# Performance work log

Hardware: AMD Instinct MI355X
Metric: run time of the kernel (lower is better)

The kernel has to match this reference:

```python
import jax, jax.numpy as jnp
import numpy as np

# Inside algorithm for a binary TreeCRF over a complete binary tree in heap
# layout: node i has children 2i+1 and 2i+2; level of size n starts at index
# n-1. Leaves are the last (n_nodes+1)//2 entries of `emissions`.
#
# Original per-node math:
#   inside[p] = logsumexp_{i,j}( em[p] + trans[p,i] + left[i] + trans[p,j] + right[j] )
# which factorizes exactly as
#   inside[p] = em[p] + logsumexp_i(trans[p,i]+left[i]) + logsumexp_j(trans[p,j]+right[j])


def setup_inputs() -> dict:
    key = jax.random.key(0)
    k1, k2 = jax.random.split(key)
    n_leaves = 131072  # 2**17
    n_nodes = 2 * n_leaves - 1  # 262143
    L = 32
    emissions = jax.random.normal(k1, (n_nodes, L), dtype=jnp.float32)
    trans = jax.random.normal(k2, (L, L), dtype=jnp.float32)
    return {"emissions": emissions, "trans": trans}


def _child_contrib(trans, child):
    # child: [n, L] inside scores of children; trans: [L, L]
    # returns [n, L]: logsumexp_c(trans[p, c] + child[:, c])
    return jax.nn.logsumexp(trans[None, :, :] + child[:, None, :], axis=2)


def reference(emissions, trans):
    n_nodes = emissions.shape[0]
    n_leaves = (n_nodes + 1) // 2
    # leaf inside scores are just the leaf emissions
    scores = emissions[n_leaves - 1:]  # [n_leaves, L]
    level = n_leaves // 2
    while level >= 1:
        # children of node (level-1)+k are scores[2k] (left) and scores[2k+1] (right)
        left = scores[0::2]   # [level, L]
        right = scores[1::2]  # [level, L]
        em = emissions[level - 1: 2 * level - 1]  # [level, L]
        scores = em + _child_contrib(trans, left) + _child_contrib(trans, right)
        level //= 2
    return scores[0]  # root inside score, [L]
```

## Files before the change

### kernel.cpp

```cpp
#include <hip/hip_runtime.h>


typedef float f32x4 __attribute__((ext_vector_type(4)));
typedef short s16x8 __attribute__((ext_vector_type(8)));
typedef short s16x4 __attribute__((ext_vector_type(4)));

#define CSTR 40

__device__ __forceinline__ short f2bf(float f) {
    unsigned u = __builtin_bit_cast(unsigned, f);
    unsigned r = (u + 0x7fffu + ((u >> 16) & 1u)) >> 16;
    return (short)r;
}

__device__ __forceinline__ float max4(float4 v) {
    return fmaxf(fmaxf(v.x, v.y), fmaxf(v.z, v.w));
}

__device__ __forceinline__ void load_afrag(const float* __restrict__ trans,
                                           int row, int kg, s16x8* a)
{
#pragma unroll
    for (int j = 0; j < 8; ++j)
        (*a)[j] = f2bf(__expf(trans[row * 32 + kg * 8 + j]));
}

template <int NC0>
__device__ __forceinline__ void wave_reduce(
    bool active, int lane,
    const float* rows, const float* __restrict__ em, int inW, int sid,
    s16x8 a0, s16x8 a1, short* C, float* M, float* outrow)
{
    constexpr int STEPS = (NC0 == 32) ? 5 : 2;
    if (active) {
        int q = lane & 31, h = lane >> 5;
        if (q < NC0) {
            const float4* src = (const float4*)(rows + q * 32 + h * 16);
            float4 x0 = src[0], x1 = src[1], x2 = src[2], x3 = src[3];
            float mm = fmaxf(fmaxf(max4(x0), max4(x1)),
                             fmaxf(max4(x2), max4(x3)));
            mm = fmaxf(mm, __shfl_xor(mm, 32));
            s16x8 w0, w1;
            w0[0] = f2bf(__expf(x0.x - mm)); w0[1] = f2bf(__expf(x0.y - mm));
            w0[2] = f2bf(__expf(x0.z - mm)); w0[3] = f2bf(__expf(x0.w - mm));
            w0[4] = f2bf(__expf(x1.x - mm)); w0[5] = f2bf(__expf(x1.y - mm));
            w0[6] = f2bf(__expf(x1.z - mm)); w0[7] = f2bf(__expf(x1.w - mm));
            w1[0] = f2bf(__expf(x2.x - mm)); w1[1] = f2bf(__expf(x2.y - mm));
            w1[2] = f2bf(__expf(x2.z - mm)); w1[3] = f2bf(__expf(x2.w - mm));
            w1[4] = f2bf(__expf(x3.x - mm)); w1[5] = f2bf(__expf(x3.y - mm));
            w1[6] = f2bf(__expf(x3.z - mm)); w1[7] = f2bf(__expf(x3.w - mm));
            *(s16x8*)(C + q * CSTR + h * 16) = w0;
            *(s16x8*)(C + q * CSTR + h * 16 + 8) = w1;
            if (h == 0) M[q] = mm;
        }
    }
    __syncthreads();
    const int ql = lane & 15, kg = lane >> 4;
    int nc = NC0;
#pragma unroll
    for (int s = 1; s <= STEPS; ++s) {
        const int Wp = inW >> s;
        const int nstr = (nc + 15) >> 4;
        for (int st = 0; st < nstr; ++st) {
            if (active) {
                int q = st * 16 + ql;
                bool valid = q < nc;
                s16x8 b = *(const s16x8*)(C + q * CSTR + kg * 8);
                f32x4 d0 = {0.f, 0.f, 0.f, 0.f};
                f32x4 d1 = {0.f, 0.f, 0.f, 0.f};
                d0 = __builtin_amdgcn_mfma_f32_16x16x32_bf16(a0, b, d0, 0, 0, 0);
                d1 = __builtin_amdgcn_mfma_f32_16x16x32_bf16(a1, b, d1, 0, 0, 0);
                float mq = M[q];
                int p = q >> 1;
                size_t node = (size_t)(Wp - 1) + (size_t)sid * (NC0 >> s) + p;
                float4 e0 = *((const float4*)(em + node * 32 + kg * 4));
                float4 e1 = *((const float4*)(em + node * 32 + 16 + kg * 4));
                float v0[4], v1[4];
#pragma unroll
                for (int r = 0; r < 4; ++r) {
                    float t0 = mq + __logf(d0[r]);
                    float t1 = mq + __logf(d1[r]);
                    v0[r] = t0 + __shfl_xor(t0, 1);
                    v1[r] = t1 + __shfl_xor(t1, 1);
                }
                v0[0] += e0.x; v0[1] += e0.y; v0[2] += e0.z; v0[3] += e0.w;
                v1[0] += e1.x; v1[1] += e1.y; v1[2] += e1.z; v1[3] += e1.w;
                if (s == STEPS) {
                    if (ql == 0) {
                        float4 o0 = {v0[0], v0[1], v0[2], v0[3]};
                        float4 o1 = {v1[0], v1[1], v1[2], v1[3]};
                        *(float4*)(outrow + kg * 4) = o0;
                        *(float4*)(outrow + 16 + kg * 4) = o1;
                    }
                } else {
                    float m2 = fmaxf(
                        fmaxf(fmaxf(v0[0], v0[1]), fmaxf(v0[2], v0[3])),
                        fmaxf(fmaxf(v1[0], v1[1]), fmaxf(v1[2], v1[3])));
                    m2 = fmaxf(m2, __shfl_xor(m2, 16));
                    m2 = fmaxf(m2, __shfl_xor(m2, 32));
                    if (valid && !(q & 1)) {
                        s16x4 u0, u1;
                        u0[0] = f2bf(__expf(v0[0] - m2));
                        u0[1] = f2bf(__expf(v0[1] - m2));
                        u0[2] = f2bf(__expf(v0[2] - m2));
                        u0[3] = f2bf(__expf(v0[3] - m2));
                        u1[0] = f2bf(__expf(v1[0] - m2));
                        u1[1] = f2bf(__expf(v1[1] - m2));
                        u1[2] = f2bf(__expf(v1[2] - m2));
                        u1[3] = f2bf(__expf(v1[3] - m2));
                        *(s16x4*)(C + p * CSTR + kg * 4) = u0;
                        *(s16x4*)(C + p * CSTR + 16 + kg * 4) = u1;
                        if (kg == 0) M[p] = m2;
                    }
                }
            }
        }
        __syncthreads();
        nc >>= 1;
    }
}

__global__ __launch_bounds__(256) void treecrf_stage(
    const float* __restrict__ rows_base, const float* __restrict__ em,
    const float* __restrict__ trans, float* __restrict__ out, int inW)
{
    __shared__ short C[4 * 32 * CSTR];
    __shared__ float M[4 * 32];
    int t = threadIdx.x, lane = t & 63, wv = t >> 6;
    int sid = blockIdx.x * 4 + wv;
    s16x8 a0, a1;
    load_afrag(trans, lane & 15, lane >> 4, &a0);
    load_afrag(trans, (lane & 15) + 16, lane >> 4, &a1);
    wave_reduce<32>(true, lane, rows_base + (size_t)sid * 1024, em, inW, sid,
                    a0, a1, C + wv * 32 * CSTR, M + wv * 32,
                    out + (size_t)sid * 32);
}

__global__ __launch_bounds__(256) void treecrf_final(
    const float* __restrict__ ws2, const float* __restrict__ em,
    const float* __restrict__ trans, float* __restrict__ out_root)
{
    __shared__ short C[4 * 32 * CSTR];
    __shared__ float M[4 * 32];
    __shared__ float R4[4 * 32];
    int t = threadIdx.x, lane = t & 63, wv = t >> 6;
    s16x8 a0, a1;
    load_afrag(trans, lane & 15, lane >> 4, &a0);
    load_afrag(trans, (lane & 15) + 16, lane >> 4, &a1);
    wave_reduce<32>(true, lane, ws2 + (size_t)wv * 1024, em, 128, wv,
                    a0, a1, C + wv * 32 * CSTR, M + wv * 32, R4 + wv * 32);
    __syncthreads();
    wave_reduce<4>(wv == 0, lane, R4, em, 4, 0, a0, a1, C, M, out_root);
}

extern "C" void kernel_launch(void* const* d_in, const int* in_sizes, int n_in,
                              void* d_out, int out_size, void* d_ws, size_t ws_size,
                              hipStream_t stream)
{
    const float* em = (const float*)d_in[0];
    const float* trans = (const float*)d_in[1];
    int n_nodes = in_sizes[0] / 32;
    int n_leaves = (n_nodes + 1) / 2;

    float* ws1 = (float*)d_ws;
    float* ws2 = ws1 + (size_t)4096 * 32;

    treecrf_stage<<<dim3(n_leaves / 128), dim3(256), 0, stream>>>(
        em + (size_t)(n_leaves - 1) * 32, em, trans, ws1, n_leaves);
    treecrf_stage<<<dim3(32), dim3(256), 0, stream>>>(
        ws1, em, trans, ws2, 4096);
    treecrf_final<<<dim3(1), dim3(256), 0, stream>>>(
        ws2, em, trans, (float*)d_out);
}
```

Baseline: 98.04 us.

## Replace block barriers with wave-local LDS waits and prefetch emissions upfront

Each wave reduces its own 32-row subtree in a private LDS slice, so the block-wide __syncthreads between levels are replaced by an s_waitcnt lgkmcnt(0) before each LDS read. All emission rows needed by every level are loaded into registers at the start, alongside the leaf rows, so global latency is no longer exposed inside the level loop. This relies on intra-wave LDS ordering for correctness and raises register pressure from the prefetched float4 arrays.

```diff
diff --git a/kernel.cpp b/kernel.cpp
--- a/kernel.cpp
+++ b/kernel.cpp
@@ -6,6 +6,7 @@
 typedef short s16x4 __attribute__((ext_vector_type(4)));
 
 #define CSTR 40
+#define LDS_WAIT() __asm__ volatile("s_waitcnt lgkmcnt(0)" ::: "memory")
 
 __device__ __forceinline__ short f2bf(float f) {
     unsigned u = __builtin_bit_cast(unsigned, f);
@@ -27,95 +28,112 @@
 
 template <int NC0>
 __device__ __forceinline__ void wave_reduce(
-    bool active, int lane,
-    const float* rows, const float* __restrict__ em, int inW, int sid,
-    s16x8 a0, s16x8 a1, short* C, float* M, float* outrow)
+    int lane, const float* rows, const float* __restrict__ em, int inW,
+    int sid, s16x8 a0, s16x8 a1, short* C, float* M, float* outrow)
 {
     constexpr int STEPS = (NC0 == 32) ? 5 : 2;
-    if (active) {
-        int q = lane & 31, h = lane >> 5;
-        if (q < NC0) {
-            const float4* src = (const float4*)(rows + q * 32 + h * 16);
-            float4 x0 = src[0], x1 = src[1], x2 = src[2], x3 = src[3];
-            float mm = fmaxf(fmaxf(max4(x0), max4(x1)),
-                             fmaxf(max4(x2), max4(x3)));
-            mm = fmaxf(mm, __shfl_xor(mm, 32));
-            s16x8 w0, w1;
-            w0[0] = f2bf(__expf(x0.x - mm)); w0[1] = f2bf(__expf(x0.y - mm));
-            w0[2] = f2bf(__expf(x0.z - mm)); w0[3] = f2bf(__expf(x0.w - mm));
-            w0[4] = f2bf(__expf(x1.x - mm)); w0[5] = f2bf(__expf(x1.y - mm));
-            w0[6] = f2bf(__expf(x1.z - mm)); w0[7] = f2bf(__expf(x1.w - mm));
-            w1[0] = f2bf(__expf(x2.x - mm)); w1[1] = f2bf(__expf(x2.y - mm));
-            w1[2] = f2bf(__expf(x2.z - mm)); w1[3] = f2bf(__expf(x2.w - mm));
-            w1[4] = f2bf(__expf(x3.x - mm)); w1[5] = f2bf(__expf(x3.y - mm));
-            w1[6] = f2bf(__expf(x3.z - mm)); w1[7] = f2bf(__expf(x3.w - mm));
-            *(s16x8*)(C + q * CSTR + h * 16) = w0;
-            *(s16x8*)(C + q * CSTR + h * 16 + 8) = w1;
-            if (h == 0) M[q] = mm;
+    constexpr int NPH = (NC0 == 32) ? 6 : 2;
+    const int ql = lane & 15, kg = lane >> 4;
+    const int q0 = lane & 31, h = lane >> 5;
+
+    float4 x0 = {0,0,0,0}, x1 = x0, x2 = x0, x3 = x0;
+    if (q0 < NC0) {
+        const float4* src = (const float4*)(rows + q0 * 32 + h * 16);
+        x0 = src[0]; x1 = src[1]; x2 = src[2]; x3 = src[3];
+    }
+
+    float4 pe0[NPH], pe1[NPH];
+    {
+        int ph = 0;
+#pragma unroll
+        for (int s = 1; s <= STEPS; ++s) {
+            const int nca = NC0 >> (s - 1);
+            const int nstr = (nca >= 16) ? (nca >> 4) : 1;
+#pragma unroll
+            for (int st = 0; st < nstr; ++st, ++ph) {
+                int p = (st * 16 + ql) >> 1;
+                size_t node = (size_t)((inW >> s) - 1)
+                            + (size_t)sid * (NC0 >> s) + p;
+                pe0[ph] = *(const float4*)(em + node * 32 + kg * 4);
+                pe1[ph] = *(const float4*)(em + node * 32 + 16 + kg * 4);
+            }
         }
     }
-    __syncthreads();
-    const int ql = lane & 15, kg = lane >> 4;
-    int nc = NC0;
+
+    if (q0 < NC0) {
+        float mm = fmaxf(fmaxf(max4(x0), max4(x1)),
+                         fmaxf(max4(x2), max4(x3)));
+        mm = fmaxf(mm, __shfl_xor(mm, 32));
+        s16x8 w0, w1;
+        w0[0] = f2bf(__expf(x0.x - mm)); w0[1] = f2bf(__expf(x0.y - mm));
+        w0[2] = f2bf(__expf(x0.z - mm)); w0[3] = f2bf(__expf(x0.w - mm));
+        w0[4] = f2bf(__expf(x1.x - mm)); w0[5] = f2bf(__expf(x1.y - mm));
+        w0[6] = f2bf(__expf(x1.z - mm)); w0[7] = f2bf(__expf(x1.w - mm));
+        w1[0] = f2bf(__expf(x2.x - mm)); w1[1] = f2bf(__expf(x2.y - mm));
+        w1[2] = f2bf(__expf(x2.z - mm)); w1[3] = f2bf(__expf(x2.w - mm));
+        w1[4] = f2bf(__expf(x3.x - mm)); w1[5] = f2bf(__expf(x3.y - mm));
+        w1[6] = f2bf(__expf(x3.z - mm)); w1[7] = f2bf(__expf(x3.w - mm));
+        *(s16x8*)(C + q0 * CSTR + h * 16) = w0;
+        *(s16x8*)(C + q0 * CSTR + h * 16 + 8) = w1;
+        if (h == 0) M[q0] = mm;
+    }
+
+    int nc = NC0, ph = 0;
 #pragma unroll
     for (int s = 1; s <= STEPS; ++s) {
-        const int Wp = inW >> s;
-        const int nstr = (nc + 15) >> 4;
-        for (int st = 0; st < nstr; ++st) {
-            if (active) {
-                int q = st * 16 + ql;
-                bool valid = q < nc;
-                s16x8 b = *(const s16x8*)(C + q * CSTR + kg * 8);
-                f32x4 d0 = {0.f, 0.f, 0.f, 0.f};
-                f32x4 d1 = {0.f, 0.f, 0.f, 0.f};
-                d0 = __builtin_amdgcn_mfma_f32_16x16x32_bf16(a0, b, d0, 0, 0, 0);
-                d1 = __builtin_amdgcn_mfma_f32_16x16x32_bf16(a1, b, d1, 0, 0, 0);
-                float mq = M[q];
-                int p = q >> 1;
-                size_t node = (size_t)(Wp - 1) + (size_t)sid * (NC0 >> s) + p;
-                float4 e0 = *((const float4*)(em + node * 32 + kg * 4));
-                float4 e1 = *((const float4*)(em + node * 32 + 16 + kg * 4));
-                float v0[4], v1[4];
+        const int nstr = (nc >= 16) ? (nc >> 4) : 1;
 #pragma unroll
-                for (int r = 0; r < 4; ++r) {
-                    float t0 = mq + __logf(d0[r]);
-                    float t1 = mq + __logf(d1[r]);
-                    v0[r] = t0 + __shfl_xor(t0, 1);
-                    v1[r] = t1 + __shfl_xor(t1, 1);
+        for (int st = 0; st < nstr; ++st, ++ph) {
+            LDS_WAIT();
+            int q = st * 16 + ql;
+            bool valid = q < nc;
+            s16x8 b = *(const s16x8*)(C + q * CSTR + kg * 8);
+            f32x4 d0 = {0.f, 0.f, 0.f, 0.f};
+            f32x4 d1 = {0.f, 0.f, 0.f, 0.f};
+            d0 = __builtin_amdgcn_mfma_f32_16x16x32_bf16(a0, b, d0, 0, 0, 0);
+            d1 = __builtin_amdgcn_mfma_f32_16x16x32_bf16(a1, b, d1, 0, 0, 0);
+            float mq = M[q];
+            int p = q >> 1;
+            float4 e0 = pe0[ph], e1 = pe1[ph];
+            float v0[4], v1[4];
+#pragma unroll
+            for (int r = 0; r < 4; ++r) {
+                float t0 = mq + __logf(d0[r]);
+                float t1 = mq + __logf(d1[r]);
+                v0[r] = t0 + __shfl_xor(t0, 1);
+                v1[r] = t1 + __shfl_xor(t1, 1);
+            }
+            v0[0] += e0.x; v0[1] += e0.y; v0[2] += e0.z; v0[3] += e0.w;
+            v1[0] += e1.x; v1[1] += e1.y; v1[2] += e1.z; v1[3] += e1.w;
+            if (s == STEPS) {
+                if (ql == 0) {
+                    float4 o0 = {v0[0], v0[1], v0[2], v0[3]};
+                    float4 o1 = {v1[0], v1[1], v1[2], v1[3]};
+                    *(float4*)(outrow + kg * 4) = o0;
+                    *(float4*)(outrow + 16 + kg * 4) = o1;
                 }
-                v0[0] += e0.x; v0[1] += e0.y; v0[2] += e0.z; v0[3] += e0.w;
-                v1[0] += e1.x; v1[1] += e1.y; v1[2] += e1.z; v1[3] += e1.w;
-                if (s == STEPS) {
-                    if (ql == 0) {
-                        float4 o0 = {v0[0], v0[1], v0[2], v0[3]};
-                        float4 o1 = {v1[0], v1[1], v1[2], v1[3]};
-                        *(float4*)(outrow + kg * 4) = o0;
-                        *(float4*)(outrow + 16 + kg * 4) = o1;
-                    }
-                } else {
-                    float m2 = fmaxf(
-                        fmaxf(fmaxf(v0[0], v0[1]), fmaxf(v0[2], v0[3])),
-                        fmaxf(fmaxf(v1[0], v1[1]), fmaxf(v1[2], v1[3])));
-                    m2 = fmaxf(m2, __shfl_xor(m2, 16));
-                    m2 = fmaxf(m2, __shfl_xor(m2, 32));
-                    if (valid && !(q & 1)) {
-                        s16x4 u0, u1;
-                        u0[0] = f2bf(__expf(v0[0] - m2));
-                        u0[1] = f2bf(__expf(v0[1] - m2));
-                        u0[2] = f2bf(__expf(v0[2] - m2));
-                        u0[3] = f2bf(__expf(v0[3] - m2));
-                        u1[0] = f2bf(__expf(v1[0] - m2));
-                        u1[1] = f2bf(__expf(v1[1] - m2));
-                        u1[2] = f2bf(__expf(v1[2] - m2));
-                        u1[3] = f2bf(__expf(v1[3] - m2));
-                        *(s16x4*)(C + p * CSTR + kg * 4) = u0;
-                        *(s16x4*)(C + p * CSTR + 16 + kg * 4) = u1;
-                        if (kg == 0) M[p] = m2;
-                    }
+            } else {
+                float m2 = fmaxf(
+                    fmaxf(fmaxf(v0[0], v0[1]), fmaxf(v0[2], v0[3])),
+                    fmaxf(fmaxf(v1[0], v1[1]), fmaxf(v1[2], v1[3])));
+                m2 = fmaxf(m2, __shfl_xor(m2, 16));
+                m2 = fmaxf(m2, __shfl_xor(m2, 32));
+                if (valid && !(q & 1)) {
+                    s16x4 u0, u1;
+                    u0[0] = f2bf(__expf(v0[0] - m2));
+                    u0[1] = f2bf(__expf(v0[1] - m2));
+                    u0[2] = f2bf(__expf(v0[2] - m2));
+                    u0[3] = f2bf(__expf(v0[3] - m2));
+                    u1[0] = f2bf(__expf(v1[0] - m2));
+                    u1[1] = f2bf(__expf(v1[1] - m2));
+                    u1[2] = f2bf(__expf(v1[2] - m2));
+                    u1[3] = f2bf(__expf(v1[3] - m2));
+                    *(s16x4*)(C + p * CSTR + kg * 4) = u0;
+                    *(s16x4*)(C + p * CSTR + 16 + kg * 4) = u1;
+                    if (kg == 0) M[p] = m2;
                 }
             }
         }
-        __syncthreads();
         nc >>= 1;
     }
 }
@@ -131,7 +149,7 @@
     s16x8 a0, a1;
     load_afrag(trans, lane & 15, lane >> 4, &a0);
     load_afrag(trans, (lane & 15) + 16, lane >> 4, &a1);
-    wave_reduce<32>(true, lane, rows_base + (size_t)sid * 1024, em, inW, sid,
+    wave_reduce<32>(lane, rows_base + (size_t)sid * 1024, em, inW, sid,
                     a0, a1, C + wv * 32 * CSTR, M + wv * 32,
                     out + (size_t)sid * 32);
 }
@@ -147,10 +165,11 @@
     s16x8 a0, a1;
     load_afrag(trans, lane & 15, lane >> 4, &a0);
     load_afrag(trans, (lane & 15) + 16, lane >> 4, &a1);
-    wave_reduce<32>(true, lane, ws2 + (size_t)wv * 1024, em, 128, wv,
+    wave_reduce<32>(lane, ws2 + (size_t)wv * 1024, em, 128, wv,
                     a0, a1, C + wv * 32 * CSTR, M + wv * 32, R4 + wv * 32);
     __syncthreads();
-    wave_reduce<4>(wv == 0, lane, R4, em, 4, 0, a0, a1, C, M, out_root);
+    if (wv == 0)
+        wave_reduce<4>(lane, R4, em, 4, 0, a0, a1, C, M, out_root);
 }
 
 extern "C" void kernel_launch(void* const* d_in, const int* in_sizes, int n_in,
```

After: 95.91 us. -2.2%, faster.
